# Performance work log

Hardware: AMD Instinct MI355X
Metric: run time of the kernel (lower is better)

The kernel has to match this reference:

```python
import jax, jax.numpy as jnp
import numpy as np

DIM = 1024
EPS = 1e-5

def layernorm(x, g, b):
    m = jnp.mean(x, axis=-1, keepdims=True)
    v = jnp.var(x, axis=-1, keepdims=True)
    return (x - m) / jnp.sqrt(v + EPS) * g + b

def setup_inputs() -> dict:
    key = jax.random.key(0)
    ks = jax.random.split(key, 12)
    B, L, D = 4, 2048, DIM
    s = 1.0 / np.sqrt(D)
    return {
        "q": jax.random.normal(ks[0], (B, L, D), jnp.float32),
        "k": jax.random.normal(ks[1], (B, L, D), jnp.float32),
        "v": jax.random.normal(ks[2], (B, L, D), jnp.float32),
        "gq": jnp.ones((D,), jnp.float32), "bq": jnp.zeros((D,), jnp.float32),
        "gk": jnp.ones((D,), jnp.float32), "bk": jnp.zeros((D,), jnp.float32),
        "gv": jnp.ones((D,), jnp.float32), "bv": jnp.zeros((D,), jnp.float32),
        "Wq": jax.random.uniform(ks[3], (D, D), jnp.float32, -s, s),
        "Wk": jax.random.uniform(ks[4], (D, D), jnp.float32, -s, s),
        "Wv": jax.random.uniform(ks[5], (D, D), jnp.float32, -s, s),
        "Wp": jax.random.uniform(ks[6], (D, D), jnp.float32, -s, s),
        "bp": jax.random.uniform(ks[7], (D,), jnp.float32, -s, s),
    }

def reference(q, k, v, gq, bq, gk, bk, gv, bv, Wq, Wk, Wv, Wp, bp):
    scale = DIM ** -0.5
    qn = layernorm(q, gq, bq) @ Wq.T  # [B,Q,D]
    kn = layernorm(k, gk, bk) @ Wk.T  # [B,K,D]
    vn = layernorm(v, gv, bv) @ Wv.T  # [B,K,D]
    attn = jnp.einsum('bqc,bkc->bqk', qn, kn)
    attn = jax.nn.relu(attn) * scale  # ReLU on raw scores, then scale (matches in-place *=)
    attn_mask = jax.nn.softmax(attn, axis=-1)
    out = jnp.einsum('bqk,bkc->bqc', attn_mask, vn)
    out = out @ Wp.T + bp
    return (attn, out)
```

## Files before the change

kernel.cpp:

```cpp
#include <hip/hip_runtime.h>


typedef __attribute__((ext_vector_type(8))) short short8v;
typedef __attribute__((ext_vector_type(4))) float f32x4;

#define DEVI __device__ __forceinline__

DEVI float b2f(unsigned short u) {
  union { unsigned int i; float f; } x;
  x.i = ((unsigned int)u) << 16;
  return x.f;
}
DEVI unsigned short f2b(float f) {
  union { float f; unsigned int i; } x;
  x.f = f;
  unsigned int r = x.i + 0x7fffu + ((x.i >> 16) & 1u);
  return (unsigned short)(r >> 16);
}

DEVI void async16(const unsigned short* g, unsigned short* l) {
  __builtin_amdgcn_global_load_lds(
      (const __attribute__((address_space(1))) void*)g,
      (__attribute__((address_space(3))) void*)l, 16, 0, 0);
}

__global__ void k_sniff(const unsigned short* __restrict__ wq, int* __restrict__ flag) {
  int tid = threadIdx.x;
  int bad = 0;
#pragma unroll
  for (int j = 0; j < 8; ++j) {
    float f = b2f(wq[tid * 8 + j]);
    bad |= (fabsf(f) > 0.0625f) ? 1 : 0;
  }
  unsigned long long m = __ballot(bad);
  if (tid == 0) *flag = (m == 0ull) ? 1 : 0;
}

struct CvtSrc { const void* p[11]; };

__global__ __launch_bounds__(256) void k_cvt(CvtSrc cs,
    unsigned short* __restrict__ wdst, unsigned short* __restrict__ vdst,
    const int* __restrict__ flag) {
  bool isbf = (*flag != 0);
  int bid = blockIdx.x;
  if (bid < 2048) {
    int s = bid >> 9;
    size_t inner = ((size_t)(bid & 511)) * 2048 + (size_t)threadIdx.x * 8;
    unsigned short* dst = wdst + (size_t)s * 1048576 + inner;
    if (isbf) {
      *(uint4*)dst = *(const uint4*)((const unsigned short*)cs.p[s] + inner);
    } else {
      const float* f = (const float*)cs.p[s] + inner;
      float4 a = *(const float4*)f;
      float4 b = *(const float4*)(f + 4);
      ushort4 o0 = { f2b(a.x), f2b(a.y), f2b(a.z), f2b(a.w) };
      ushort4 o1 = { f2b(b.x), f2b(b.y), f2b(b.z), f2b(b.w) };
      *(ushort4*)dst = o0;
      *(ushort4*)(dst + 4) = o1;
    }
  } else {
    size_t idx = ((size_t)(bid - 2048)) * 2048 + (size_t)threadIdx.x * 8;
    if (idx < 7168) {
      int vsel = (int)(idx >> 10);
      size_t pos = idx & 1023;
      unsigned short* dst = vdst + idx;
      if (isbf) {
        *(uint4*)dst = *(const uint4*)((const unsigned short*)cs.p[4 + vsel] + pos);
      } else {
        const float* f = (const float*)cs.p[4 + vsel] + pos;
        float4 a = *(const float4*)f;
        float4 b = *(const float4*)(f + 4);
        ushort4 o0 = { f2b(a.x), f2b(a.y), f2b(a.z), f2b(a.w) };
        ushort4 o1 = { f2b(b.x), f2b(b.y), f2b(b.z), f2b(b.w) };
        *(ushort4*)dst = o0;
        *(ushort4*)(dst + 4) = o1;
      }
    }
  }
}

__global__ __launch_bounds__(256) void k_ln(
    const void* __restrict__ q, const void* __restrict__ k, const void* __restrict__ v,
    const unsigned short* __restrict__ vecs, const int* __restrict__ flag,
    unsigned short* __restrict__ xn) {
  int row = blockIdx.x;
  int t = row >> 13;
  size_t r = (size_t)(row & 8191);
  const void* src = (t == 0) ? q : (t == 1) ? k : v;
  int tid = threadIdx.x;
  float x0, x1, x2, x3;
  if (*flag) {
    const unsigned short* p = (const unsigned short*)src + r * 1024 + (size_t)tid * 4;
    ushort4 pk = *(const ushort4*)p;
    x0 = b2f(pk.x); x1 = b2f(pk.y); x2 = b2f(pk.z); x3 = b2f(pk.w);
  } else {
    const float* p = (const float*)src + r * 1024 + (size_t)tid * 4;
    float4 pk = *(const float4*)p;
    x0 = pk.x; x1 = pk.y; x2 = pk.z; x3 = pk.w;
  }
  float s1 = x0 + x1 + x2 + x3;
  float s2 = x0 * x0 + x1 * x1 + x2 * x2 + x3 * x3;
  for (int off = 32; off > 0; off >>= 1) {
    s1 += __shfl_down(s1, off);
    s2 += __shfl_down(s2, off);
  }
  __shared__ float sh[8];
  if ((tid & 63) == 0) { sh[tid >> 6] = s1; sh[4 + (tid >> 6)] = s2; }
  __syncthreads();
  float m  = (sh[0] + sh[1] + sh[2] + sh[3]) * (1.0f / 1024.0f);
  float m2 = (sh[4] + sh[5] + sh[6] + sh[7]) * (1.0f / 1024.0f);
  float rstd = rsqrtf(m2 - m * m + 1e-5f);
  const unsigned short* g = vecs + t * 2048 + tid * 4;
  ushort4 gv = *(const ushort4*)g;
  ushort4 bb = *(const ushort4*)(g + 1024);
  ushort4 o;
  o.x = f2b((x0 - m) * rstd * b2f(gv.x) + b2f(bb.x));
  o.y = f2b((x1 - m) * rstd * b2f(gv.y) + b2f(bb.y));
  o.z = f2b((x2 - m) * rstd * b2f(gv.z) + b2f(bb.z));
  o.w = f2b((x3 - m) * rstd * b2f(gv.w) + b2f(bb.w));
  *(ushort4*)(xn + (size_t)row * 1024 + (size_t)tid * 4) = o;
}

__global__ __launch_bounds__(256) void k_softmax(const void* __restrict__ S,
    unsigned short* __restrict__ P, const int* __restrict__ flag) {
  size_t row = blockIdx.x;
  int tid = threadIdx.x;
  float v[8];
  if (*flag) {
    const unsigned short* s = (const unsigned short*)S + row * 2048 + (size_t)tid * 8;
    ushort4 a = *(const ushort4*)s;
    ushort4 b = *(const ushort4*)(s + 4);
    v[0] = b2f(a.x); v[1] = b2f(a.y); v[2] = b2f(a.z); v[3] = b2f(a.w);
    v[4] = b2f(b.x); v[5] = b2f(b.y); v[6] = b2f(b.z); v[7] = b2f(b.w);
  } else {
    const float* s = (const float*)S + row * 2048 + (size_t)tid * 8;
    float4 a = *(const float4*)s;
    float4 b = *(const float4*)(s + 4);
    v[0] = a.x; v[1] = a.y; v[2] = a.z; v[3] = a.w;
    v[4] = b.x; v[5] = b.y; v[6] = b.z; v[7] = b.w;
  }
  float mx = v[0];
#pragma unroll
  for (int j = 1; j < 8; ++j) mx = fmaxf(mx, v[j]);
  for (int off = 32; off > 0; off >>= 1) mx = fmaxf(mx, __shfl_down(mx, off));
  __shared__ float sh[8];
  if ((tid & 63) == 0) sh[tid >> 6] = mx;
  __syncthreads();
  mx = fmaxf(fmaxf(sh[0], sh[1]), fmaxf(sh[2], sh[3]));
  float sum = 0.f;
#pragma unroll
  for (int j = 0; j < 8; ++j) { v[j] = __expf(v[j] - mx); sum += v[j]; }
  for (int off = 32; off > 0; off >>= 1) sum += __shfl_down(sum, off);
  if ((tid & 63) == 0) sh[4 + (tid >> 6)] = sum;
  __syncthreads();
  float inv = 1.0f / (sh[4] + sh[5] + sh[6] + sh[7]);
  ushort4 o0 = { f2b(v[0] * inv), f2b(v[1] * inv), f2b(v[2] * inv), f2b(v[3] * inv) };
  ushort4 o1 = { f2b(v[4] * inv), f2b(v[5] * inv), f2b(v[6] * inv), f2b(v[7] * inv) };
  unsigned short* p = P + row * 2048 + (size_t)tid * 8;
  *(ushort4*)p = o0;
  *(ushort4*)(p + 4) = o1;
}

template <int EPI>
__global__ __launch_bounds__(256) void k_gemm(
    const unsigned short* __restrict__ A, const unsigned short* __restrict__ B,
    void* __restrict__ Cv, long long coff,
    int K, int lda, int ldb, int ldc, int ldct,
    long long sAb, long long sBb, long long sCb,
    float scale, const unsigned short* __restrict__ bias,
    const int* __restrict__ flag) {
  __shared__ __align__(16) unsigned short sA[128 * 64];
  __shared__ __align__(16) unsigned short sB[128 * 64];
  const unsigned short* Ab = A + (long long)blockIdx.z * sAb;
  const unsigned short* Bb = B + (long long)blockIdx.z * sBb;
  long long cbase = coff + (long long)blockIdx.z * sCb;
  int m0 = blockIdx.y * 128, n0 = blockIdx.x * 128;
  int tid = threadIdx.x;
  int lane = tid & 63;
  int w = tid >> 6;
  int wm = w & 1, wn = w >> 1;
  int l15 = lane & 15, quad = lane >> 4;

  int r8 = lane >> 3;
  int scol = ((lane & 7) ^ r8) * 8;
  int srow0 = w * 32 + r8;
  const unsigned short* gA = Ab + (size_t)(m0 + srow0) * lda + scol;
  const unsigned short* gB = Bb + (size_t)(n0 + srow0) * ldb + scol;
  unsigned short* lA = &sA[(size_t)(w * 32) * 64];
  unsigned short* lB = &sB[(size_t)(w * 32) * 64];

  int rxor = l15 & 7;
  const unsigned short* rA = &sA[(size_t)(wm * 64 + l15) * 64];
  const unsigned short* rB = &sB[(size_t)(wn * 64 + l15) * 64];

  f32x4 acc[4][4];
#pragma unroll
  for (int i = 0; i < 4; ++i)
#pragma unroll
    for (int j = 0; j < 4; ++j) acc[i][j] = (f32x4){0.f, 0.f, 0.f, 0.f};

  for (int k0 = 0; k0 < K; k0 += 64) {
#pragma unroll
    for (int j = 0; j < 4; ++j)
      async16(gA + (size_t)(j * 8) * lda + k0, lA + j * 8 * 64);
#pragma unroll
    for (int j = 0; j < 4; ++j)
      async16(gB + (size_t)(j * 8) * ldb + k0, lB + j * 8 * 64);
    __syncthreads();
#pragma unroll
    for (int c = 0; c < 2; ++c) {
      int col = ((c * 4 + quad) ^ rxor) * 8;
      short8v af[4], bf[4];
#pragma unroll
      for (int i = 0; i < 4; ++i) {
        af[i] = *(const short8v*)(rA + i * 1024 + col);
        bf[i] = *(const short8v*)(rB + i * 1024 + col);
      }
#pragma unroll
      for (int mt = 0; mt < 4; ++mt)
#pragma unroll
        for (int nt = 0; nt < 4; ++nt)
          acc[mt][nt] = __builtin_amdgcn_mfma_f32_16x16x32_bf16(af[mt], bf[nt], acc[mt][nt], 0, 0, 0);
    }
    __syncthreads();
  }

  bool isbf = (EPI == 1 || EPI == 3) ? (*flag != 0) : true;
#pragma unroll
  for (int mt = 0; mt < 4; ++mt) {
    int mb = m0 + wm * 64 + mt * 16 + quad * 4;
#pragma unroll
    for (int nt = 0; nt < 4; ++nt) {
      int n = n0 + wn * 64 + nt * 16 + l15;
      f32x4 vc = acc[mt][nt];
      if (EPI == 2) {
        unsigned short* Ct = (unsigned short*)Cv + cbase;
        ushort4 o = { f2b(vc[0]), f2b(vc[1]), f2b(vc[2]), f2b(vc[3]) };
        *(ushort4*)&Ct[(size_t)n * ldct + mb] = o;
      } else if (EPI == 0) {
        unsigned short* C = (unsigned short*)Cv + cbase;
#pragma unroll
        for (int r2 = 0; r2 < 4; ++r2) C[(size_t)(mb + r2) * ldc + n] = f2b(vc[r2]);
      } else if (EPI == 1) {
        if (isbf) {
          unsigned short* C = (unsigned short*)Cv + cbase;
#pragma unroll
          for (int r2 = 0; r2 < 4; ++r2)
            C[(size_t)(mb + r2) * ldc + n] = f2b(fmaxf(vc[r2], 0.f) * scale);
        } else {
          float* C = (float*)Cv + cbase;
#pragma unroll
          for (int r2 = 0; r2 < 4; ++r2)
            C[(size_t)(mb + r2) * ldc + n] = fmaxf(vc[r2], 0.f) * scale;
        }
      } else {
        float bv2 = b2f(bias[n]);
        if (isbf) {
          unsigned short* C = (unsigned short*)Cv + cbase;
#pragma unroll
          for (int r2 = 0; r2 < 4; ++r2) C[(size_t)(mb + r2) * ldc + n] = f2b(vc[r2] + bv2);
        } else {
          float* C = (float*)Cv + cbase;
#pragma unroll
          for (int r2 = 0; r2 < 4; ++r2) C[(size_t)(mb + r2) * ldc + n] = vc[r2] + bv2;
        }
      }
    }
  }
}

static const size_t MB_ = 1024 * 1024;
static const size_t OFF_W   = 0;
static const size_t OFF_VEC = 8 * MB_;
static const size_t OFF_FLG = 8 * MB_ + 64 * 1024;
static const size_t OFF_XN  = 8 * MB_ + 128 * 1024;
static const size_t OFF_QN  = OFF_XN + 48 * MB_;
static const size_t OFF_KN  = OFF_QN + 16 * MB_;
static const size_t OFF_VNT = OFF_KN + 16 * MB_;
static const size_t OFF_P   = OFF_XN;
static const size_t OFF_O1  = OFF_XN + 32 * MB_;

extern "C" void kernel_launch(void* const* d_in, const int* in_sizes, int n_in,
                              void* d_out, int out_size, void* d_ws, size_t ws_size,
                              hipStream_t stream) {
  (void)in_sizes; (void)n_in; (void)out_size; (void)ws_size;
  char* ws = (char*)d_ws;
  unsigned short* Wb  = (unsigned short*)(ws + OFF_W);
  unsigned short* Vec = (unsigned short*)(ws + OFF_VEC);
  int*            Flg = (int*)(ws + OFF_FLG);
  unsigned short* XN  = (unsigned short*)(ws + OFF_XN);
  unsigned short* QN  = (unsigned short*)(ws + OFF_QN);
  unsigned short* VNT = (unsigned short*)(ws + OFF_VNT);
  unsigned short* P   = (unsigned short*)(ws + OFF_P);
  unsigned short* O1  = (unsigned short*)(ws + OFF_O1);

  k_sniff<<<1, 64, 0, stream>>>((const unsigned short*)d_in[9], Flg);

  CvtSrc cs;
  cs.p[0] = d_in[9];  cs.p[1] = d_in[10]; cs.p[2] = d_in[11]; cs.p[3] = d_in[12];
  cs.p[4] = d_in[3];  cs.p[5] = d_in[4];  cs.p[6] = d_in[5];  cs.p[7] = d_in[6];
  cs.p[8] = d_in[7];  cs.p[9] = d_in[8];  cs.p[10] = d_in[13];
  k_cvt<<<2052, 256, 0, stream>>>(cs, Wb, Vec, Flg);

  k_ln<<<24576, 256, 0, stream>>>(d_in[0], d_in[1], d_in[2], Vec, Flg, XN);

  k_gemm<0><<<dim3(8, 64, 2), 256, 0, stream>>>(
      XN, Wb, QN,
      0,
      1024, 1024, 1024, 1024, 0,
      8388608LL, 1048576LL, 8388608LL,
      0.f, nullptr, Flg);
  k_gemm<2><<<dim3(8, 16, 4), 256, 0, stream>>>(
      XN + 2 * 8388608, Wb + 2 * 1048576, VNT,
      0,
      1024, 1024, 1024, 0, 2048,
      (long long)2048 * 1024, 0LL, (long long)1024 * 2048,
      0.f, nullptr, Flg);
  k_gemm<1><<<dim3(16, 16, 4), 256, 0, stream>>>(
      QN, QN + 8388608, d_out,
      0,
      1024, 1024, 1024, 2048, 0,
      (long long)2048 * 1024, (long long)2048 * 1024,
      (long long)2048 * 2048,
      0.03125f, nullptr, Flg);
  k_softmax<<<8192, 256, 0, stream>>>(d_out, P, Flg);
  k_gemm<0><<<dim3(8, 16, 4), 256, 0, stream>>>(
      P, VNT, O1,
      0,
      2048, 2048, 2048, 1024, 0,
      (long long)2048 * 2048, (long long)1024 * 2048,
      (long long)2048 * 1024,
      0.f, nullptr, Flg);
  k_gemm<3><<<dim3(8, 64, 1), 256, 0, stream>>>(
      O1, Wb + 3 * 1048576, d_out,
      16777216,
      1024, 1024, 1024, 1024, 0,
      0LL, 0LL, 0LL,
      0.f, Vec + 6144, Flg);
}
```

Measured before the change: 436.9 us.

## Fuse sniff/convert/layernorm into one prep kernel and merge projection GEMMs

Replaces the separate dtype-sniff, weight-convert and layernorm kernels with a single prep kernel where every block re-sniffs the dtype inline instead of reading a flag written by another launch. The Q/K and V-transposed projection GEMMs are merged into one launch. The PV GEMM now uses a narrower 128x64 tile to double its block count. The aim is to cut launch count and improve occupancy for the under-filled PV GEMM. The cost is redundant sniff loads in every block and a smaller tile with less reuse for the PV GEMM.

```diff
diff --git a/kernel.cpp b/kernel.cpp
--- a/kernel.cpp
+++ b/kernel.cpp
@@ -18,39 +18,82 @@
   return (unsigned short)(r >> 16);
 }
 
+DEVI bool sniff_bf16(const unsigned short* wq) {
+  int bad = 0;
+#pragma unroll
+  for (int j = 0; j < 64; ++j) bad |= (fabsf(b2f(wq[j])) > 0.0625f) ? 1 : 0;
+  return bad == 0;
+}
+
 DEVI void async16(const unsigned short* g, unsigned short* l) {
   __builtin_amdgcn_global_load_lds(
       (const __attribute__((address_space(1))) void*)g,
       (__attribute__((address_space(3))) void*)l, 16, 0, 0);
 }
 
-__global__ void k_sniff(const unsigned short* __restrict__ wq, int* __restrict__ flag) {
-  int tid = threadIdx.x;
-  int bad = 0;
-#pragma unroll
-  for (int j = 0; j < 8; ++j) {
-    float f = b2f(wq[tid * 8 + j]);
-    bad |= (fabsf(f) > 0.0625f) ? 1 : 0;
-  }
-  unsigned long long m = __ballot(bad);
-  if (tid == 0) *flag = (m == 0ull) ? 1 : 0;
-}
-
-struct CvtSrc { const void* p[11]; };
-
-__global__ __launch_bounds__(256) void k_cvt(CvtSrc cs,
-    unsigned short* __restrict__ wdst, unsigned short* __restrict__ vdst,
-    const int* __restrict__ flag) {
-  bool isbf = (*flag != 0);
-  int bid = blockIdx.x;
+template <int NT>
+DEVI void gemm_core(unsigned short* sA, unsigned short* sB,
+                    const unsigned short* Ab, const unsigned short* Bb,
+                    int m0, int n0, int lda, int ldb, int K, int tid,
+                    f32x4 (&acc)[4][NT]) {
+  const int BN = NT * 32;
+  int lane = tid & 63, w = tid >> 6;
+  int l15 = lane & 15, quad = lane >> 4;
+  int r8 = lane >> 3;
+  int scol = ((lane & 7) ^ r8) * 8;
+  const unsigned short* gA = Ab + (size_t)(m0 + w * 32 + r8) * lda + scol;
+  const unsigned short* gB = Bb + (size_t)(n0 + w * (BN / 4) + r8) * ldb + scol;
+  unsigned short* lA = &sA[(size_t)(w * 32) * 64];
+  unsigned short* lB = &sB[(size_t)(w * (BN / 4)) * 64];
+  int wm = w & 1, wn = w >> 1;
+  int rxor = l15 & 7;
+  const unsigned short* rA = &sA[(size_t)(wm * 64 + l15) * 64];
+  const unsigned short* rB = &sB[(size_t)(wn * (BN / 2) + l15) * 64];
+
+  for (int k0 = 0; k0 < K; k0 += 64) {
+#pragma unroll
+    for (int j = 0; j < 4; ++j)
+      async16(gA + (size_t)(j * 8) * lda + k0, lA + j * 8 * 64);
+#pragma unroll
+    for (int j = 0; j < NT; ++j)
+      async16(gB + (size_t)(j * 8) * ldb + k0, lB + j * 8 * 64);
+    __syncthreads();
+#pragma unroll
+    for (int c = 0; c < 2; ++c) {
+      int col = ((c * 4 + quad) ^ rxor) * 8;
+      short8v af[4], bf[NT];
+#pragma unroll
+      for (int i = 0; i < 4; ++i) af[i] = *(const short8v*)(rA + i * 1024 + col);
+#pragma unroll
+      for (int i = 0; i < NT; ++i) bf[i] = *(const short8v*)(rB + i * 1024 + col);
+#pragma unroll
+      for (int mt = 0; mt < 4; ++mt)
+#pragma unroll
+        for (int nt = 0; nt < NT; ++nt)
+          acc[mt][nt] = __builtin_amdgcn_mfma_f32_16x16x32_bf16(af[mt], bf[nt], acc[mt][nt], 0, 0, 0);
+    }
+    __syncthreads();
+  }
+}
+
+struct PrepArgs {
+  const void* q; const void* k; const void* v;
+  const void* g[3]; const void* b[3];
+  const void* W[4];
+};
+
+__global__ __launch_bounds__(256) void k_prep(PrepArgs pa,
+    unsigned short* __restrict__ Wb, unsigned short* __restrict__ XN) {
+  bool isbf = sniff_bf16((const unsigned short*)pa.W[0]);
+  int bid = blockIdx.x, tid = threadIdx.x;
   if (bid < 2048) {
     int s = bid >> 9;
-    size_t inner = ((size_t)(bid & 511)) * 2048 + (size_t)threadIdx.x * 8;
-    unsigned short* dst = wdst + (size_t)s * 1048576 + inner;
+    size_t inner = ((size_t)(bid & 511)) * 2048 + (size_t)tid * 8;
+    unsigned short* dst = Wb + (size_t)s * 1048576 + inner;
     if (isbf) {
-      *(uint4*)dst = *(const uint4*)((const unsigned short*)cs.p[s] + inner);
+      *(uint4*)dst = *(const uint4*)((const unsigned short*)pa.W[s] + inner);
     } else {
-      const float* f = (const float*)cs.p[s] + inner;
+      const float* f = (const float*)pa.W[s] + inner;
       float4 a = *(const float4*)f;
       float4 b = *(const float4*)(f + 4);
       ushort4 o0 = { f2b(a.x), f2b(a.y), f2b(a.z), f2b(a.w) };
@@ -59,74 +102,177 @@
       *(ushort4*)(dst + 4) = o1;
     }
   } else {
-    size_t idx = ((size_t)(bid - 2048)) * 2048 + (size_t)threadIdx.x * 8;
-    if (idx < 7168) {
-      int vsel = (int)(idx >> 10);
-      size_t pos = idx & 1023;
-      unsigned short* dst = vdst + idx;
-      if (isbf) {
-        *(uint4*)dst = *(const uint4*)((const unsigned short*)cs.p[4 + vsel] + pos);
+    int row = bid - 2048;
+    int t = row >> 13;
+    size_t r = (size_t)(row & 8191);
+    const void* src = (t == 0) ? pa.q : (t == 1) ? pa.k : pa.v;
+    float x0, x1, x2, x3;
+    if (isbf) {
+      ushort4 pk = *(const ushort4*)((const unsigned short*)src + r * 1024 + (size_t)tid * 4);
+      x0 = b2f(pk.x); x1 = b2f(pk.y); x2 = b2f(pk.z); x3 = b2f(pk.w);
+    } else {
+      float4 pk = *(const float4*)((const float*)src + r * 1024 + (size_t)tid * 4);
+      x0 = pk.x; x1 = pk.y; x2 = pk.z; x3 = pk.w;
+    }
+    float s1 = x0 + x1 + x2 + x3;
+    float s2 = x0 * x0 + x1 * x1 + x2 * x2 + x3 * x3;
+    for (int off = 32; off > 0; off >>= 1) {
+      s1 += __shfl_down(s1, off);
+      s2 += __shfl_down(s2, off);
+    }
+    __shared__ float sh[8];
+    if ((tid & 63) == 0) { sh[tid >> 6] = s1; sh[4 + (tid >> 6)] = s2; }
+    __syncthreads();
+    float m  = (sh[0] + sh[1] + sh[2] + sh[3]) * (1.0f / 1024.0f);
+    float m2 = (sh[4] + sh[5] + sh[6] + sh[7]) * (1.0f / 1024.0f);
+    float rstd = rsqrtf(m2 - m * m + 1e-5f);
+    float g0, g1, g2, g3, c0, c1, c2, c3;
+    if (isbf) {
+      ushort4 gv = *(const ushort4*)((const unsigned short*)pa.g[t] + tid * 4);
+      ushort4 bb = *(const ushort4*)((const unsigned short*)pa.b[t] + tid * 4);
+      g0 = b2f(gv.x); g1 = b2f(gv.y); g2 = b2f(gv.z); g3 = b2f(gv.w);
+      c0 = b2f(bb.x); c1 = b2f(bb.y); c2 = b2f(bb.z); c3 = b2f(bb.w);
+    } else {
+      float4 gv = *(const float4*)((const float*)pa.g[t] + tid * 4);
+      float4 bb = *(const float4*)((const float*)pa.b[t] + tid * 4);
+      g0 = gv.x; g1 = gv.y; g2 = gv.z; g3 = gv.w;
+      c0 = bb.x; c1 = bb.y; c2 = bb.z; c3 = bb.w;
+    }
+    ushort4 o;
+    o.x = f2b((x0 - m) * rstd * g0 + c0);
+    o.y = f2b((x1 - m) * rstd * g1 + c1);
+    o.z = f2b((x2 - m) * rstd * g2 + c2);
+    o.w = f2b((x3 - m) * rstd * g3 + c3);
+    *(ushort4*)(XN + (size_t)row * 1024 + (size_t)tid * 4) = o;
+  }
+}
+
+__global__ __launch_bounds__(256) void k_megaproj(
+    const unsigned short* __restrict__ XN, const unsigned short* __restrict__ Wb,
+    unsigned short* __restrict__ QN, unsigned short* __restrict__ VNT) {
+  __shared__ __align__(16) unsigned short sA[128 * 64];
+  __shared__ __align__(16) unsigned short sB[128 * 64];
+  int x = blockIdx.x, tid = threadIdx.x;
+  int lane = tid & 63, w = tid >> 6;
+  int wm = w & 1, wn = w >> 1;
+  int l15 = lane & 15, quad = lane >> 4;
+  f32x4 acc[4][4];
+#pragma unroll
+  for (int i = 0; i < 4; ++i)
+#pragma unroll
+    for (int j = 0; j < 4; ++j) acc[i][j] = (f32x4){0.f, 0.f, 0.f, 0.f};
+
+  if (x < 1024) {
+    int t = x >> 9, i = x & 511;
+    int m0 = (i >> 3) * 128, n0 = (i & 7) * 128;
+    gemm_core<4>(sA, sB, XN + (size_t)t * 8388608, Wb + (size_t)t * 1048576,
+                 m0, n0, 1024, 1024, 1024, tid, acc);
+    unsigned short* C = QN + (size_t)t * 8388608;
+#pragma unroll
+    for (int mt = 0; mt < 4; ++mt) {
+      int mb = m0 + wm * 64 + mt * 16 + quad * 4;
+#pragma unroll
+      for (int nt = 0; nt < 4; ++nt) {
+        int n = n0 + wn * 64 + nt * 16 + l15;
+        f32x4 vc = acc[mt][nt];
+#pragma unroll
+        for (int r2 = 0; r2 < 4; ++r2) C[(size_t)(mb + r2) * 1024 + n] = f2b(vc[r2]);
+      }
+    }
+  } else {
+    int i = x - 1024, z = i >> 7, j = i & 127;
+    int m0 = (j >> 3) * 128, n0 = (j & 7) * 128;
+    gemm_core<4>(sA, sB, XN + 2 * 8388608 + (size_t)z * 2097152,
+                 Wb + 2 * 1048576, m0, n0, 1024, 1024, 1024, tid, acc);
+    unsigned short* Ct = VNT + (size_t)z * 2097152;
+#pragma unroll
+    for (int mt = 0; mt < 4; ++mt) {
+      int mb = m0 + wm * 64 + mt * 16 + quad * 4;
+#pragma unroll
+      for (int nt = 0; nt < 4; ++nt) {
+        int n = n0 + wn * 64 + nt * 16 + l15;
+        f32x4 vc = acc[mt][nt];
+        ushort4 o = { f2b(vc[0]), f2b(vc[1]), f2b(vc[2]), f2b(vc[3]) };
+        *(ushort4*)&Ct[(size_t)n * 2048 + mb] = o;
+      }
+    }
+  }
+}
+
+template <int EPI, int NT>
+__global__ __launch_bounds__(256) void k_gemm(
+    const unsigned short* __restrict__ A, const unsigned short* __restrict__ B,
+    void* __restrict__ Cv, long long coff,
+    int K, int lda, int ldb, int ldc,
+    long long sAb, long long sBb, long long sCb,
+    float scale, const void* __restrict__ bias,
+    const unsigned short* __restrict__ wq_sniff) {
+  __shared__ __align__(16) unsigned short sA[128 * 64];
+  __shared__ __align__(16) unsigned short sB[NT * 32 * 64];
+  const int BN = NT * 32;
+  int tid = threadIdx.x;
+  int lane = tid & 63, w = tid >> 6;
+  int wm = w & 1, wn = w >> 1;
+  int l15 = lane & 15, quad = lane >> 4;
+  int m0 = blockIdx.y * 128, n0 = blockIdx.x * BN;
+  f32x4 acc[4][NT];
+#pragma unroll
+  for (int i = 0; i < 4; ++i)
+#pragma unroll
+    for (int j = 0; j < NT; ++j) acc[i][j] = (f32x4){0.f, 0.f, 0.f, 0.f};
+
+  gemm_core<NT>(sA, sB, A + (long long)blockIdx.z * sAb,
+                B + (long long)blockIdx.z * sBb, m0, n0, lda, ldb, K, tid, acc);
+
+  long long cbase = coff + (long long)blockIdx.z * sCb;
+  bool isbf = (EPI != 0) ? sniff_bf16(wq_sniff) : true;
+#pragma unroll
+  for (int mt = 0; mt < 4; ++mt) {
+    int mb = m0 + wm * 64 + mt * 16 + quad * 4;
+#pragma unroll
+    for (int nt = 0; nt < NT; ++nt) {
+      int n = n0 + wn * (BN / 2) + nt * 16 + l15;
+      f32x4 vc = acc[mt][nt];
+      if (EPI == 0) {
+        unsigned short* C = (unsigned short*)Cv + cbase;
+#pragma unroll
+        for (int r2 = 0; r2 < 4; ++r2) C[(size_t)(mb + r2) * ldc + n] = f2b(vc[r2]);
+      } else if (EPI == 1) {
+        if (isbf) {
+          unsigned short* C = (unsigned short*)Cv + cbase;
+#pragma unroll
+          for (int r2 = 0; r2 < 4; ++r2)
+            C[(size_t)(mb + r2) * ldc + n] = f2b(fmaxf(vc[r2], 0.f) * scale);
+        } else {
+          float* C = (float*)Cv + cbase;
+#pragma unroll
+          for (int r2 = 0; r2 < 4; ++r2)
+            C[(size_t)(mb + r2) * ldc + n] = fmaxf(vc[r2], 0.f) * scale;
+        }
       } else {
-        const float* f = (const float*)cs.p[4 + vsel] + pos;
-        float4 a = *(const float4*)f;
-        float4 b = *(const float4*)(f + 4);
-        ushort4 o0 = { f2b(a.x), f2b(a.y), f2b(a.z), f2b(a.w) };
-        ushort4 o1 = { f2b(b.x), f2b(b.y), f2b(b.z), f2b(b.w) };
-        *(ushort4*)dst = o0;
-        *(ushort4*)(dst + 4) = o1;
+        float bv2 = isbf ? b2f(((const unsigned short*)bias)[n])
+                         : ((const float*)bias)[n];
+        if (isbf) {
+          unsigned short* C = (unsigned short*)Cv + cbase;
+#pragma unroll
+          for (int r2 = 0; r2 < 4; ++r2) C[(size_t)(mb + r2) * ldc + n] = f2b(vc[r2] + bv2);
+        } else {
+          float* C = (float*)Cv + cbase;
+#pragma unroll
+          for (int r2 = 0; r2 < 4; ++r2) C[(size_t)(mb + r2) * ldc + n] = vc[r2] + bv2;
+        }
       }
     }
   }
 }
 
-__global__ __launch_bounds__(256) void k_ln(
-    const void* __restrict__ q, const void* __restrict__ k, const void* __restrict__ v,
-    const unsigned short* __restrict__ vecs, const int* __restrict__ flag,
-    unsigned short* __restrict__ xn) {
-  int row = blockIdx.x;
-  int t = row >> 13;
-  size_t r = (size_t)(row & 8191);
-  const void* src = (t == 0) ? q : (t == 1) ? k : v;
-  int tid = threadIdx.x;
-  float x0, x1, x2, x3;
-  if (*flag) {
-    const unsigned short* p = (const unsigned short*)src + r * 1024 + (size_t)tid * 4;
-    ushort4 pk = *(const ushort4*)p;
-    x0 = b2f(pk.x); x1 = b2f(pk.y); x2 = b2f(pk.z); x3 = b2f(pk.w);
-  } else {
-    const float* p = (const float*)src + r * 1024 + (size_t)tid * 4;
-    float4 pk = *(const float4*)p;
-    x0 = pk.x; x1 = pk.y; x2 = pk.z; x3 = pk.w;
-  }
-  float s1 = x0 + x1 + x2 + x3;
-  float s2 = x0 * x0 + x1 * x1 + x2 * x2 + x3 * x3;
-  for (int off = 32; off > 0; off >>= 1) {
-    s1 += __shfl_down(s1, off);
-    s2 += __shfl_down(s2, off);
-  }
-  __shared__ float sh[8];
-  if ((tid & 63) == 0) { sh[tid >> 6] = s1; sh[4 + (tid >> 6)] = s2; }
-  __syncthreads();
-  float m  = (sh[0] + sh[1] + sh[2] + sh[3]) * (1.0f / 1024.0f);
-  float m2 = (sh[4] + sh[5] + sh[6] + sh[7]) * (1.0f / 1024.0f);
-  float rstd = rsqrtf(m2 - m * m + 1e-5f);
-  const unsigned short* g = vecs + t * 2048 + tid * 4;
-  ushort4 gv = *(const ushort4*)g;
-  ushort4 bb = *(const ushort4*)(g + 1024);
-  ushort4 o;
-  o.x = f2b((x0 - m) * rstd * b2f(gv.x) + b2f(bb.x));
-  o.y = f2b((x1 - m) * rstd * b2f(gv.y) + b2f(bb.y));
-  o.z = f2b((x2 - m) * rstd * b2f(gv.z) + b2f(bb.z));
-  o.w = f2b((x3 - m) * rstd * b2f(gv.w) + b2f(bb.w));
-  *(ushort4*)(xn + (size_t)row * 1024 + (size_t)tid * 4) = o;
-}
-
 __global__ __launch_bounds__(256) void k_softmax(const void* __restrict__ S,
-    unsigned short* __restrict__ P, const int* __restrict__ flag) {
+    unsigned short* __restrict__ P, const unsigned short* __restrict__ wq_sniff) {
+  bool isbf = sniff_bf16(wq_sniff);
   size_t row = blockIdx.x;
   int tid = threadIdx.x;
   float v[8];
-  if (*flag) {
+  if (isbf) {
     const unsigned short* s = (const unsigned short*)S + row * 2048 + (size_t)tid * 8;
     ushort4 a = *(const ushort4*)s;
     ushort4 b = *(const ushort4*)(s + 4);
@@ -161,122 +307,11 @@
   *(ushort4*)(p + 4) = o1;
 }
 
-template <int EPI>
-__global__ __launch_bounds__(256) void k_gemm(
-    const unsigned short* __restrict__ A, const unsigned short* __restrict__ B,
-    void* __restrict__ Cv, long long coff,
-    int K, int lda, int ldb, int ldc, int ldct,
-    long long sAb, long long sBb, long long sCb,
-    float scale, const unsigned short* __restrict__ bias,
-    const int* __restrict__ flag) {
-  __shared__ __align__(16) unsigned short sA[128 * 64];
-  __shared__ __align__(16) unsigned short sB[128 * 64];
-  const unsigned short* Ab = A + (long long)blockIdx.z * sAb;
-  const unsigned short* Bb = B + (long long)blockIdx.z * sBb;
-  long long cbase = coff + (long long)blockIdx.z * sCb;
-  int m0 = blockIdx.y * 128, n0 = blockIdx.x * 128;
-  int tid = threadIdx.x;
-  int lane = tid & 63;
-  int w = tid >> 6;
-  int wm = w & 1, wn = w >> 1;
-  int l15 = lane & 15, quad = lane >> 4;
-
-  int r8 = lane >> 3;
-  int scol = ((lane & 7) ^ r8) * 8;
-  int srow0 = w * 32 + r8;
-  const unsigned short* gA = Ab + (size_t)(m0 + srow0) * lda + scol;
-  const unsigned short* gB = Bb + (size_t)(n0 + srow0) * ldb + scol;
-  unsigned short* lA = &sA[(size_t)(w * 32) * 64];
-  unsigned short* lB = &sB[(size_t)(w * 32) * 64];
-
-  int rxor = l15 & 7;
-  const unsigned short* rA = &sA[(size_t)(wm * 64 + l15) * 64];
-  const unsigned short* rB = &sB[(size_t)(wn * 64 + l15) * 64];
-
-  f32x4 acc[4][4];
-#pragma unroll
-  for (int i = 0; i < 4; ++i)
-#pragma unroll
-    for (int j = 0; j < 4; ++j) acc[i][j] = (f32x4){0.f, 0.f, 0.f, 0.f};
-
-  for (int k0 = 0; k0 < K; k0 += 64) {
-#pragma unroll
-    for (int j = 0; j < 4; ++j)
-      async16(gA + (size_t)(j * 8) * lda + k0, lA + j * 8 * 64);
-#pragma unroll
-    for (int j = 0; j < 4; ++j)
-      async16(gB + (size_t)(j * 8) * ldb + k0, lB + j * 8 * 64);
-    __syncthreads();
-#pragma unroll
-    for (int c = 0; c < 2; ++c) {
-      int col = ((c * 4 + quad) ^ rxor) * 8;
-      short8v af[4], bf[4];
-#pragma unroll
-      for (int i = 0; i < 4; ++i) {
-        af[i] = *(const short8v*)(rA + i * 1024 + col);
-        bf[i] = *(const short8v*)(rB + i * 1024 + col);
-      }
-#pragma unroll
-      for (int mt = 0; mt < 4; ++mt)
-#pragma unroll
-        for (int nt = 0; nt < 4; ++nt)
-          acc[mt][nt] = __builtin_amdgcn_mfma_f32_16x16x32_bf16(af[mt], bf[nt], acc[mt][nt], 0, 0, 0);
-    }
-    __syncthreads();
-  }
-
-  bool isbf = (EPI == 1 || EPI == 3) ? (*flag != 0) : true;
-#pragma unroll
-  for (int mt = 0; mt < 4; ++mt) {
-    int mb = m0 + wm * 64 + mt * 16 + quad * 4;
-#pragma unroll
-    for (int nt = 0; nt < 4; ++nt) {
-      int n = n0 + wn * 64 + nt * 16 + l15;
-      f32x4 vc = acc[mt][nt];
-      if (EPI == 2) {
-        unsigned short* Ct = (unsigned short*)Cv + cbase;
-        ushort4 o = { f2b(vc[0]), f2b(vc[1]), f2b(vc[2]), f2b(vc[3]) };
-        *(ushort4*)&Ct[(size_t)n * ldct + mb] = o;
-      } else if (EPI == 0) {
-        unsigned short* C = (unsigned short*)Cv + cbase;
-#pragma unroll
-        for (int r2 = 0; r2 < 4; ++r2) C[(size_t)(mb + r2) * ldc + n] = f2b(vc[r2]);
-      } else if (EPI == 1) {
-        if (isbf) {
-          unsigned short* C = (unsigned short*)Cv + cbase;
-#pragma unroll
-          for (int r2 = 0; r2 < 4; ++r2)
-            C[(size_t)(mb + r2) * ldc + n] = f2b(fmaxf(vc[r2], 0.f) * scale);
-        } else {
-          float* C = (float*)Cv + cbase;
-#pragma unroll
-          for (int r2 = 0; r2 < 4; ++r2)
-            C[(size_t)(mb + r2) * ldc + n] = fmaxf(vc[r2], 0.f) * scale;
-        }
-      } else {
-        float bv2 = b2f(bias[n]);
-        if (isbf) {
-          unsigned short* C = (unsigned short*)Cv + cbase;
-#pragma unroll
-          for (int r2 = 0; r2 < 4; ++r2) C[(size_t)(mb + r2) * ldc + n] = f2b(vc[r2] + bv2);
-        } else {
-          float* C = (float*)Cv + cbase;
-#pragma unroll
-          for (int r2 = 0; r2 < 4; ++r2) C[(size_t)(mb + r2) * ldc + n] = vc[r2] + bv2;
-        }
-      }
-    }
-  }
-}
-
 static const size_t MB_ = 1024 * 1024;
 static const size_t OFF_W   = 0;
-static const size_t OFF_VEC = 8 * MB_;
-static const size_t OFF_FLG = 8 * MB_ + 64 * 1024;
 static const size_t OFF_XN  = 8 * MB_ + 128 * 1024;
 static const size_t OFF_QN  = OFF_XN + 48 * MB_;
-static const size_t OFF_KN  = OFF_QN + 16 * MB_;
-static const size_t OFF_VNT = OFF_KN + 16 * MB_;
+static const size_t OFF_VNT = OFF_QN + 32 * MB_;
 static const size_t OFF_P   = OFF_XN;
 static const size_t OFF_O1  = OFF_XN + 32 * MB_;
 
@@ -286,55 +321,44 @@
   (void)in_sizes; (void)n_in; (void)out_size; (void)ws_size;
   char* ws = (char*)d_ws;
   unsigned short* Wb  = (unsigned short*)(ws + OFF_W);
-  unsigned short* Vec = (unsigned short*)(ws + OFF_VEC);
-  int*            Flg = (int*)(ws + OFF_FLG);
   unsigned short* XN  = (unsigned short*)(ws + OFF_XN);
   unsigned short* QN  = (unsigned short*)(ws + OFF_QN);
   unsigned short* VNT = (unsigned short*)(ws + OFF_VNT);
   unsigned short* P   = (unsigned short*)(ws + OFF_P);
   unsigned short* O1  = (unsigned short*)(ws + OFF_O1);
-
-  k_sniff<<<1, 64, 0, stream>>>((const unsigned short*)d_in[9], Flg);
-
-  CvtSrc cs;
-  cs.p[0] = d_in[9];  cs.p[1] = d_in[10]; cs.p[2] = d_in[11]; cs.p[3] = d_in[12];
-  cs.p[4] = d_in[3];  cs.p[5] = d_in[4];  cs.p[6] = d_in[5];  cs.p[7] = d_in[6];
-  cs.p[8] = d_in[7];  cs.p[9] = d_in[8];  cs.p[10] = d_in[13];
-  k_cvt<<<2052, 256, 0, stream>>>(cs, Wb, Vec, Flg);
-
-  k_ln<<<24576, 256, 0, stream>>>(d_in[0], d_in[1], d_in[2], Vec, Flg, XN);
-
-  k_gemm<0><<<dim3(8, 64, 2), 256, 0, stream>>>(
-      XN, Wb, QN,
-      0,
-      1024, 1024, 1024, 1024, 0,
-      8388608LL, 1048576LL, 8388608LL,
-      0.f, nullptr, Flg);
-  k_gemm<2><<<dim3(8, 16, 4), 256, 0, stream>>>(
-      XN + 2 * 8388608, Wb + 2 * 1048576, VNT,
-      0,
-      1024, 1024, 1024, 0, 2048,
-      (long long)2048 * 1024, 0LL, (long long)1024 * 2048,
-      0.f, nullptr, Flg);
-  k_gemm<1><<<dim3(16, 16, 4), 256, 0, stream>>>(
+  const unsigned short* WqS = (const unsigned short*)d_in[9];
+
+  PrepArgs pa;
+  pa.q = d_in[0]; pa.k = d_in[1]; pa.v = d_in[2];
+  pa.g[0] = d_in[3]; pa.b[0] = d_in[4];
+  pa.g[1] = d_in[5]; pa.b[1] = d_in[6];
+  pa.g[2] = d_in[7]; pa.b[2] = d_in[8];
+  pa.W[0] = d_in[9]; pa.W[1] = d_in[10]; pa.W[2] = d_in[11]; pa.W[3] = d_in[12];
+
+  k_prep<<<26624, 256, 0, stream>>>(pa, Wb, XN);
+
+  k_megaproj<<<1536, 256, 0, stream>>>(XN, Wb, QN, VNT);
+
+  k_gemm<1, 4><<<dim3(16, 16, 4), 256, 0, stream>>>(
       QN, QN + 8388608, d_out,
       0,
-      1024, 1024, 1024, 2048, 0,
-      (long long)2048 * 1024, (long long)2048 * 1024,
-      (long long)2048 * 2048,
-      0.03125f, nullptr, Flg);
-  k_softmax<<<8192, 256, 0, stream>>>(d_out, P, Flg);
-  k_gemm<0><<<dim3(8, 16, 4), 256, 0, stream>>>(
+      1024, 1024, 1024, 2048,
+      2097152LL, 2097152LL, 4194304LL,
+      0.03125f, nullptr, WqS);
+
+  k_softmax<<<8192, 256, 0, stream>>>(d_out, P, WqS);
+
+  k_gemm<0, 2><<<dim3(16, 16, 4), 256, 0, stream>>>(
       P, VNT, O1,
       0,
-      2048, 2048, 2048, 1024, 0,
-      (long long)2048 * 2048, (long long)1024 * 2048,
-      (long long)2048 * 1024,
-      0.f, nullptr, Flg);
-  k_gemm<3><<<dim3(8, 64, 1), 256, 0, stream>>>(
+      2048, 2048, 2048, 1024,
+      4194304LL, 2097152LL, 2097152LL,
+      0.f, nullptr, WqS);
+
+  k_gemm<3, 4><<<dim3(8, 64, 1), 256, 0, stream>>>(
       O1, Wb + 3 * 1048576, d_out,
       16777216,
-      1024, 1024, 1024, 1024, 0,
+      1024, 1024, 1024, 1024,
       0LL, 0LL, 0LL,
-      0.f, Vec + 6144, Flg);
-}
+      0.f, d_in[13], WqS);
+}
```

Result: no change. 429.9 us (-1.6%).
